# Kernel optimization log

Measured on AMD Instinct MI355X. Metric: run time of the kernel, lower is better.

Reference implementation:

```python
import jax, jax.numpy as jnp
from jax import lax
import numpy as np

B, N, G, K = 4, 1024, 128, 32
D_MODEL, DEPTH, CLS = 384, 12, 40
D_INNER, D_STATE, D_CONV, DT_RANK = 768, 16, 4, 24
EPS = 1e-5
BN_SCALE = 1.0 / float(np.sqrt(1.0 + EPS))  # eval BN, running_mean=0, running_var=1


def layernorm(x, w, b):
    mu = x.mean(-1, keepdims=True)
    var = ((x - mu) ** 2).mean(-1, keepdims=True)
    return (x - mu) * lax.rsqrt(var + EPS) * w + b


def bn_eval(x, g, b):
    return x * (g * BN_SCALE) + b


def fps(xyz, n):
    Bb, Nn, _ = xyz.shape
    first = jnp.zeros((Bb,), jnp.int32)

    def step(carry, _):
        dmin, last = carry
        p = jnp.take_along_axis(xyz, last[:, None, None], axis=1)  # B,1,3
        dmin = jnp.minimum(dmin, jnp.sum((xyz - p) ** 2, -1))
        nxt = jnp.argmax(dmin, -1).astype(jnp.int32)
        return (dmin, nxt), nxt

    _, rest = lax.scan(step, (jnp.full((Bb, Nn), 1e10, xyz.dtype), first), None, length=n - 1)
    return jnp.concatenate([first[None, :], rest], 0).T  # B,G


def group_points(xyz):
    idx = fps(xyz, G)
    center = jnp.take_along_axis(xyz, idx[:, :, None], axis=1)            # B,G,3
    d2 = jnp.sum((center[:, :, None, :] - xyz[:, None, :, :]) ** 2, -1)   # B,G,N
    _, knn = lax.top_k(-d2, K)                                            # B,G,K
    nb = jax.vmap(lambda p, i: p[i])(xyz, knn)                            # B,G,K,3
    return nb - center[:, :, None, :], center


def encoder(pg, w1, b1, g1, bb1, w2, b2, w3, b3, g2, bb2, w4, b4):
    Bb, Gg, Kk, _ = pg.shape
    f = pg.reshape(Bb * Gg, Kk, 3)
    f = jax.nn.relu(bn_eval(f @ w1.T + b1, g1, bb1))                      # BG,K,128
    f = f @ w2.T + b2                                                     # BG,K,256
    fg = f.max(1, keepdims=True)
    f = jnp.concatenate([jnp.broadcast_to(fg, f.shape), f], -1)           # BG,K,512
    f = jax.nn.relu(bn_eval(f @ w3.T + b3, g2, bb2))
    f = f @ w4.T + b4
    return f.max(1).reshape(Bb, Gg, -1)                                   # B,G,C


def mamba_mixer(x, ipw, cw, cb, xpw, dpw, dpb, A_log, Dp, opw):
    L = x.shape[1]
    xz = x @ ipw.T                                                        # B,L,2*Di
    u, z = jnp.split(xz, 2, -1)
    up = jnp.pad(u, ((0, 0), (D_CONV - 1, 0), (0, 0)))                    # causal depthwise conv
    u = sum(up[:, k:k + L, :] * cw[:, k] for k in range(D_CONV)) + cb
    u = jax.nn.silu(u)
    xdb = u @ xpw.T
    dt, Bm, Cm = jnp.split(xdb, [DT_RANK, DT_RANK + D_STATE], -1)
    dt = jax.nn.softplus(dt @ dpw.T + dpb)                                # B,L,Di
    A = -jnp.exp(A_log)                                                   # Di,Ds

    def step(h, inp):
        dt_t, B_t, C_t, u_t = inp
        h = jnp.exp(dt_t[:, :, None] * A) * h + (dt_t * u_t)[:, :, None] * B_t[:, None, :]
        return h, jnp.einsum('bds,bs->bd', h, C_t)

    h0 = jnp.zeros((x.shape[0], D_INNER, D_STATE), x.dtype)
    _, ys = lax.scan(step, h0, (dt.swapaxes(0, 1), Bm.swapaxes(0, 1), Cm.swapaxes(0, 1), u.swapaxes(0, 1)))
    y = ys.swapaxes(0, 1) + u * Dp
    return (y * jax.nn.silu(z)) @ opw.T


def forward(pts, enc_w1, enc_b1, enc_bn1_g, enc_bn1_b, enc_w2, enc_b2, enc_w3, enc_b3,
            enc_bn2_g, enc_bn2_b, enc_w4, enc_b4, pos_w1, pos_b1, pos_w2, pos_b2,
            ln_w, ln_b, in_proj_w, conv_w, conv_b, x_proj_w, dt_proj_w, dt_proj_b,
            A_log, D_param, out_proj_w, normf_w, normf_b, norm_w, norm_b,
            head_w1, head_b1, head_bn1_g, head_bn1_b, head_w2, head_b2,
            head_bn2_g, head_bn2_b, head_w3, head_b3):
    nb, center = group_points(pts)
    tok = encoder(nb, enc_w1, enc_b1, enc_bn1_g, enc_bn1_b, enc_w2, enc_b2,
                  enc_w3, enc_b3, enc_bn2_g, enc_bn2_b, enc_w4, enc_b4)    # B,G,384
    pos = jax.nn.gelu(center @ pos_w1.T + pos_b1, approximate=False) @ pos_w2.T + pos_b2

    # PointMamba token reordering: sort by center x, y, z and concatenate -> L = 3G
    toks, poss = [], []
    for ax in range(3):
        o = jnp.argsort(center[:, :, ax], axis=-1)[:, :, None]
        toks.append(jnp.take_along_axis(tok, o, axis=1))
        poss.append(jnp.take_along_axis(pos, o, axis=1))
    tok = jnp.concatenate(toks, 1)
    pos = jnp.concatenate(poss, 1)

    h = tok + pos
    res = jnp.zeros_like(h)

    def layer_step(carry, p):
        h, res = carry
        lnw, lnb, ipw, cw, cb, xpw, dpw, dpb, Al, Dp, opw = p
        res = h + res
        x = layernorm(res, lnw, lnb)
        h = mamba_mixer(x, ipw, cw, cb, xpw, dpw, dpb, Al, Dp, opw)
        return (h, res), None

    (h, res), _ = lax.scan(layer_step, (h, res),
                           (ln_w, ln_b, in_proj_w, conv_w, conv_b, x_proj_w,
                            dt_proj_w, dt_proj_b, A_log, D_param, out_proj_w))
    x = layernorm(h + res, normf_w, normf_b)   # MixerModel.norm_f
    x = layernorm(x, norm_w, norm_b)           # PointMamba.norm
    feat = x.mean(1)                           # B,384
    h1 = jax.nn.relu(bn_eval(feat @ head_w1.T + head_b1, head_bn1_g, head_bn1_b))
    h2 = jax.nn.relu(bn_eval(h1 @ head_w2.T + head_b2, head_bn2_g, head_bn2_b))
    return h2 @ head_w3.T + head_b3            # B,CLS


def setup_inputs():
    key = jax.random.key(0)
    ks = iter(jax.random.split(key, 64))

    def rn(shape, s=0.02):
        return jax.random.normal(next(ks), shape, jnp.float32) * s

    inp = dict(
        pts=jax.random.normal(next(ks), (B, N, 3), jnp.float32),
        enc_w1=rn((128, 3), 0.1), enc_b1=jnp.zeros((128,)),
        enc_bn1_g=jnp.ones((128,)), enc_bn1_b=jnp.zeros((128,)),
        enc_w2=rn((256, 128), 0.05), enc_b2=jnp.zeros((256,)),
        enc_w3=rn((512, 512), 0.05), enc_b3=jnp.zeros((512,)),
        enc_bn2_g=jnp.ones((512,)), enc_bn2_b=jnp.zeros((512,)),
        enc_w4=rn((D_MODEL, 512), 0.05), enc_b4=jnp.zeros((D_MODEL,)),
        pos_w1=rn((128, 3), 0.1), pos_b1=jnp.zeros((128,)),
        pos_w2=rn((D_MODEL, 128), 0.05), pos_b2=jnp.zeros((D_MODEL,)),
        ln_w=jnp.ones((DEPTH, D_MODEL)), ln_b=jnp.zeros((DEPTH, D_MODEL)),
        in_proj_w=rn((DEPTH, 2 * D_INNER, D_MODEL)),
        conv_w=rn((DEPTH, D_INNER, D_CONV), 0.2), conv_b=jnp.zeros((DEPTH, D_INNER)),
        x_proj_w=rn((DEPTH, DT_RANK + 2 * D_STATE, D_INNER)),
        dt_proj_w=rn((DEPTH, D_INNER, DT_RANK), 0.1),
        dt_proj_b=jnp.full((DEPTH, D_INNER), -4.6, jnp.float32),
        A_log=jnp.broadcast_to(jnp.log(jnp.arange(1, D_STATE + 1, dtype=jnp.float32)),
                               (DEPTH, D_INNER, D_STATE)).copy(),
        D_param=jnp.ones((DEPTH, D_INNER)),
        out_proj_w=rn((DEPTH, D_MODEL, D_INNER)),
        normf_w=jnp.ones((D_MODEL,)), normf_b=jnp.zeros((D_MODEL,)),
        norm_w=jnp.ones((D_MODEL,)), norm_b=jnp.zeros((D_MODEL,)),
        head_w1=rn((256, D_MODEL), 0.05), head_b1=jnp.zeros((256,)),
        head_bn1_g=jnp.ones((256,)), head_bn1_b=jnp.zeros((256,)),
        head_w2=rn((256, 256), 0.05), head_b2=jnp.zeros((256,)),
        head_bn2_g=jnp.ones((256,)), head_bn2_b=jnp.zeros((256,)),
        head_w3=rn((CLS, 256), 0.05), head_b3=jnp.zeros((CLS,)),
    )
    return inp


def reference(pts, enc_w1, enc_b1, enc_bn1_g, enc_bn1_b, enc_w2, enc_b2, enc_w3, enc_b3,
              enc_bn2_g, enc_bn2_b, enc_w4, enc_b4, pos_w1, pos_b1, pos_w2, pos_b2,
              ln_w, ln_b, in_proj_w, conv_w, conv_b, x_proj_w, dt_proj_w, dt_proj_b,
              A_log, D_param, out_proj_w, normf_w, normf_b, norm_w, norm_b,
              head_w1, head_b1, head_bn1_g, head_bn1_b, head_w2, head_b2,
              head_bn2_g, head_bn2_b, head_w3, head_b3):
    return forward(pts, enc_w1, enc_b1, enc_bn1_g, enc_bn1_b, enc_w2, enc_b2, enc_w3, enc_b3,
                   enc_bn2_g, enc_bn2_b, enc_w4, enc_b4, pos_w1, pos_b1, pos_w2, pos_b2,
                   ln_w, ln_b, in_proj_w, conv_w, conv_b, x_proj_w, dt_proj_w, dt_proj_b,
                   A_log, D_param, out_proj_w, normf_w, normf_b, norm_w, norm_b,
                   head_w1, head_b1, head_bn1_g, head_bn1_b, head_w2, head_b2,
                   head_bn2_g, head_bn2_b, head_w3, head_b3)
```

## Files before the change

### kernel.cpp

```cpp
#include <hip/hip_runtime.h>
#include <hip/hip_bf16.h>

using bf16 = __hip_bfloat16;
using short8  = __attribute__((ext_vector_type(8))) short;
using floatx4 = __attribute__((ext_vector_type(4))) float;
using ull = unsigned long long;

constexpr int Bn = 4, Np = 1024, Gn = 128, Kn = 32;
constexpr int DM = 384, DEPTH = 12, CLSn = 40;
constexpr int DI = 768, DSt = 16, DTR = 24;
constexpr int Ln = 384;
constexpr int NCH = 12, CHS = 32;
constexpr int CHB = 8,  NCB = 48;
constexpr int XDBS = 1536*56;
constexpr int MC = 4096;
constexpr float EPSf = 1e-5f;
constexpr float BNS = 0.99999500003749968752f;
constexpr float LOG2E = 1.4426950408889634f;

static __device__ __forceinline__ short f2bf(float f){
  bf16 h = __float2bfloat16(f);
  return *reinterpret_cast<short*>(&h);
}
static __device__ __forceinline__ float fsig(float x){ return 1.f/(1.f + __expf(-x)); }
static __device__ __forceinline__ float fsoftplus(float x){
  return fmaxf(x, 0.f) + __logf(1.f + __expf(-fabsf(x)));
}
static __device__ __forceinline__ ull umax64(ull a, ull b){ return a > b ? a : b; }

template<int CTRL>
static __device__ __forceinline__ int dppmov(int x){
  return __builtin_amdgcn_update_dpp(0, x, CTRL, 0xF, 0xF, true);
}
static __device__ __forceinline__ ull redmax64(ull key){
  #define RSTEP(CTRL) { \
    int hi = (int)(unsigned)(key >> 32), lo = (int)(unsigned)key; \
    int h2 = dppmov<CTRL>(hi), l2 = dppmov<CTRL>(lo); \
    ull k2 = ((ull)(unsigned)h2 << 32) | (unsigned)l2; \
    if (k2 > key) key = k2; }
  RSTEP(0x111) RSTEP(0x112) RSTEP(0x114) RSTEP(0x118) RSTEP(0x142) RSTEP(0x143)
  #undef RSTEP
  return key;
}

__global__ __launch_bounds__(256) void front_kernel(const float* __restrict__ pts,
    float* __restrict__ center,
    const float* __restrict__ s0, const float* __restrict__ s1,
    const float* __restrict__ s2, const float* __restrict__ s3,
    const float* __restrict__ s4, const float* __restrict__ s5,
    bf16* __restrict__ dst){
  __shared__ float4 P[1024];
  __shared__ ull red[2][4];
  if (blockIdx.x >= Bn){
    long i = ((long)(blockIdx.x - Bn)*256 + threadIdx.x)*4;
    if (i >= 11624448L) return;
    const float* s; long off;
    if      (i <  7077888L){ s = s0; off = 0L; }
// ... 587 lines not shown
  for (int i = 0; i < 6; ++i){ int c = ln + 64*i; float t = hr[c] + rr[c]; rr[c] = t; v[i] = t; s += t; }
  #pragma unroll
  for (int o = 32; o > 0; o >>= 1) s += __shfl_xor(s, o);
  float mu = s * (1.f/DM);
  float q = 0.f;
  #pragma unroll
  for (int i = 0; i < 6; ++i){ float d = v[i] - mu; q += d*d; }
  #pragma unroll
  for (int o = 32; o > 0; o >>= 1) q += __shfl_xor(q, o);
  float rstd = rsqrtf(q * (1.f/DM) + EPSf);
  #pragma unroll
  for (int i = 0; i < 6; ++i){ int c = ln + 64*i;
    xr[c] = __float2bfloat16((v[i]-mu)*rstd*w[c] + bias[c]); }
}

__global__ __launch_bounds__(256) void scanA_big(const float* __restrict__ xz,
    const float* __restrict__ xdbp, int nks,
    const float* __restrict__ cw, const float* __restrict__ cb,
    const float* __restrict__ dpw, const float* __restrict__ dpb,
    const float* __restrict__ A_log,
    float* __restrict__ SB_S, float* __restrict__ SB_dt,
    float* __restrict__ xdbR){
  __shared__ float sRow[CHB*56];
  int blk = blockIdx.x;
  int c = blk % NCB; int bd = blk / NCB; int dch = bd % 3; int b = bd / 3;
  int t = threadIdx.x; int d = dch*256 + t;
  int l0 = c*CHB;
  for (int i = t; i < CHB*56; i += 256){
    size_t base = ((size_t)(b*Ln + l0))*56 + i;
    float s = xdbp[base];
    for (int k = 1; k < nks; ++k) s += xdbp[(size_t)k*XDBS + base];
    sRow[i] = s;
    if (dch == 0) xdbR[base] = s;
  }
  float xv[CHB+3];
  #pragma unroll
  for (int j = 0; j < 3; ++j){
    int ll = l0 - 3 + j;
    xv[j] = (ll >= 0) ? xz[((size_t)(b*Ln + ll))*1536 + d] : 0.f;
  }
  const float* xp = xz + ((size_t)(b*Ln + l0))*1536 + d;
  #pragma unroll
  for (int i = 0; i < CHB; ++i) xv[3+i] = xp[(size_t)i*1536];
  float cw0 = cw[d*4+0], cw1 = cw[d*4+1], cw2 = cw[d*4+2], cw3 = cw[d*4+3];
  float cbv = cb[d];
  float uu[CHB];
  #pragma unroll
  for (int i = 0; i < CHB; ++i){
    float v = xv[i]*cw0 + xv[i+1]*cw1 + xv[i+2]*cw2 + xv[i+3]*cw3 + cbv;
    uu[i] = v * fsig(v);
  }
  float w[DTR];
  const float* wp = dpw + (size_t)d*DTR;
  #pragma unroll
  for (int j = 0; j < DTR; ++j) w[j] = wp[j];
  float a2[DSt], h[DSt];
  const float* ap = A_log + (size_t)d*DSt;
  #pragma unroll
  for (int s = 0; s < DSt; ++s){ a2[s] = -__expf(ap[s]) * LOG2E; h[s] = 0.f; }
  float dbias = dpb[d];
  float sumdt = 0.f;
  __syncthreads();
  for (int i = 0; i < CHB; ++i){
    int ro = i*56;
    float dtr = dbias;
    #pragma unroll
    for (int j = 0; j < DTR; ++j) dtr += w[j] * sRow[ro + j];
    float dtv = fsoftplus(dtr);
    sumdt += dtv;
    float du = dtv * uu[i];
    #pragma unroll
    for (int s = 0; s < DSt; ++s)
      h[s] = exp2f(dtv * a2[s]) * h[s] + du * sRow[ro + 24 + s];
  }
  size_t sb = ((size_t)blk*256 + t)*16;
  #pragma unroll
  for (int s = 0; s < DSt; ++s) SB_S[sb + s] = h[s];
  SB_dt[(size_t)blk*256 + t] = sumdt;
}

__global__ __launch_bounds__(256) void prefix_kernel(const float* __restrict__ A_log,
    const float* __restrict__ SB_S, const float* __restrict__ SB_dt,
    float* __restrict__ H0){
  int bb = blockIdx.x;
  int bd = bb >> 4;
  int dch = bd % 3;
  int tt = threadIdx.x;
  int tloc = tt >> 4, s = tt & 15;
  int t = (bb & 15)*16 + tloc;
  int d = dch*256 + t;
  float a2 = -__expf(A_log[(size_t)d*DSt + s]) * LOG2E;
  float H = 0.f;
  size_t tb = ((size_t)bd*NCB)*256 + t;
  for (int c = 0; c < NCB; ++c){
    size_t base = (tb + (size_t)c*256)*16 + s;
    H0[base] = H;
    float sd = SB_dt[tb + (size_t)c*256];
    H = exp2f(sd * a2) * H + SB_S[base];
  }
}

__global__ __launch_bounds__(256) void scanB_big(const float* __restrict__ xz,
    const float* __restrict__ xdbR,
    const float* __restrict__ cw, const float* __restrict__ cb,
    const float* __restrict__ dpw, const float* __restrict__ dpb,
    const float* __restrict__ A_log, const float* __restrict__ Dp,
    const float* __restrict__ H0, bf16* __restrict__ yb){
  __shared__ float sRow[CHB*56];
  int blk = blockIdx.x;
  int c = blk % NCB; int bd = blk / NCB; int dch = bd % 3; int b = bd / 3;
  int t = threadIdx.x; int d = dch*256 + t;
  int l0 = c*CHB;
  for (int i = t; i < CHB*56; i += 256)
    sRow[i] = xdbR[((size_t)(b*Ln + l0))*56 + i];
  float xv[CHB+3];
  #pragma unroll
  for (int j = 0; j < 3; ++j){
    int ll = l0 - 3 + j;
    xv[j] = (ll >= 0) ? xz[((size_t)(b*Ln + ll))*1536 + d] : 0.f;
  }
  const float* xp = xz + ((size_t)(b*Ln + l0))*1536 + d;
  #pragma unroll
  for (int i = 0; i < CHB; ++i) xv[3+i] = xp[(size_t)i*1536];
  float cw0 = cw[d*4+0], cw1 = cw[d*4+1], cw2 = cw[d*4+2], cw3 = cw[d*4+3];
  float cbv = cb[d];
  float uu[CHB];
  #pragma unroll
  for (int i = 0; i < CHB; ++i){
    float v = xv[i]*cw0 + xv[i+1]*cw1 + xv[i+2]*cw2 + xv[i+3]*cw3 + cbv;
    uu[i] = v * fsig(v);
  }
  float w[DTR];
  const float* wp = dpw + (size_t)d*DTR;
  #pragma unroll
  for (int j = 0; j < DTR; ++j) w[j] = wp[j];
  float a2[DSt], h[DSt];
  const float* ap = A_log + (size_t)d*DSt;
  #pragma unroll
  for (int s = 0; s < DSt; ++s) a2[s] = -__expf(ap[s]) * LOG2E;
  size_t hbase = (((size_t)bd*NCB + c)*256 + t)*16;
  #pragma unroll
  for (int s = 0; s < DSt; ++s) h[s] = H0[hbase + s];
  float dbias = dpb[d];
  float Dd = Dp[d];
  const float* zrow = xz + ((size_t)(b*Ln + l0))*1536 + 768 + d;
  bf16* ybr = yb + ((size_t)(b*Ln + l0))*DI + d;
  __syncthreads();
  for (int i = 0; i < CHB; ++i){
    int ro = i*56;
    float dtr = dbias;
    #pragma unroll
    for (int j = 0; j < DTR; ++j) dtr += w[j] * sRow[ro + j];
    float dtv = fsoftplus(dtr);
    float u = uu[i];
    float du = dtv * u;
    float yv = 0.f;
    #pragma unroll
    for (int s = 0; s < DSt; ++s){
      h[s] = exp2f(dtv * a2[s]) * h[s] + du * sRow[ro + 24 + s];
      yv += h[s] * sRow[ro + 40 + s];
    }
    float yfull = yv + u*Dd;
    float zv = zrow[(size_t)i*1536];
    ybr[(size_t)i*DI] = __float2bfloat16(yfull * (zv * fsig(zv)));
  }
}

__global__ __launch_bounds__(256) void scanA_kernel(const float* __restrict__ xz,
                                                    const float* __restrict__ xdbp, int nks,
                                                    const float* __restrict__ cw,
                                                    const float* __restrict__ cb,
                                                    const float* __restrict__ dpw,
                                                    const float* __restrict__ dpb,
                                                    const float* __restrict__ A_log,
                                                    float* __restrict__ SB_S,
                                                    float* __restrict__ SB_dt,
                                                    float* __restrict__ BND){
  __shared__ float sRow[CHS*56];
  __shared__ float sU[CHS*256];
  int blk = blockIdx.x;
  int c = blk % NCH; int bd = blk / NCH; int dch = bd % 3; int b = bd / 3;
  int t = threadIdx.x; int d = dch*256 + t;
// ... 199 lines not shown
    h1[t] = fmaxf(a, 0.f);
  }
  __syncthreads();
  {
    float a = b2[t];
    #pragma unroll 4
    for (int j = 0; j < 256; ++j) a += w2[(size_t)t*256 + j] * h1[j];
    a = a * (g2[t] * BNS) + bb2[t];
    h2[t] = fmaxf(a, 0.f);
  }
  __syncthreads();
  if (t < CLSn){
    float a = b3[t];
    for (int j = 0; j < 256; ++j) a += w3[(size_t)t*256 + j] * h2[j];
    out[b*CLSn + t] = a;
  }
}

extern "C" void kernel_launch(void* const* d_in, const int* in_sizes, int n_in,
                              void* d_out, int out_size, void* d_ws, size_t ws_size,
                              hipStream_t stream) {
  if (n_in < 42) return;
  if (out_size < Bn*CLSn) return;
  constexpr size_t WS_FLOATS = 3919936;
  if (ws_size < WS_FLOATS * sizeof(float)) return;
  constexpr size_t MIDF = 5812224;
  constexpr size_t BIGF = 9437184;
  const bool mid = ws_size >= (WS_FLOATS + MIDF) * sizeof(float);
  const bool big = ws_size >= (WS_FLOATS + MIDF + BIGF) * sizeof(float);

// ... 22 lines not shown
  const float* head_w3   = (const float*)d_in[40]; const float* head_b3   = (const float*)d_in[41];

  float* ws = (float*)d_ws;
  float* hb   = ws;
  float* resb = ws + 589824;
  float* U    = ws + 1179648;
  float* center = U;
  float* nb     = U + 1536;
  float* tok    = U + 50688;
  int*   order  = (int*)(U + 247296);
  bf16*  F3b_s  = (bf16*)(U + 262144);
  bf16*  F3c_s  = (bf16*)(U + 1310720);
  float* xz   = U;
  float* xdb  = U + 2359296;
  bf16*  xb   = (bf16*)(U + 2445312);
  float* SBdt = U + 2445312;
  float* BND  = U + 2482176;
  float* SBS  = hb;
  float* xf   = U;
  float* featp = U + 589824;
  float* WB = ws + WS_FLOATS;
  bf16* wb_ip = (bf16*)WB;
  bf16* wb_op = (bf16*)(WB + 3538944);
  bf16* wb_xp = (bf16*)(WB + 5308416);
  bf16* wb_e2 = (bf16*)(WB + 5566464);
  bf16* wb_e3 = (bf16*)(WB + 5582848);
  bf16* wb_e4 = (bf16*)(WB + 5713920);
  float* BIGB = WB + MIDF;
  bf16*  F3bB = (bf16*)BIGB;
  bf16*  F3cB = (bf16*)(BIGB + 4194304);
  float* xdbp_b = BIGB;
  float* xdbR   = BIGB + 1032192;
  bf16*  yb     = (bf16*)(BIGB + 1118208);
  float* SBS_b  = BIGB + 1708032;
  float* H0b    = BIGB + 4067328;
  float* SBdt_b = BIGB + 6426624;

  front_kernel<<<mid ? (Bn + 11352) : Bn, 256, 0, stream>>>(pts, center,
      in_proj_w, out_proj_w, x_proj_w, enc_w2, enc_w3, enc_w4, (bf16*)WB);
  knn_kernel<<<Bn*Gn, 256, 0, stream>>>(pts, center, nb);

  if (big){
    enc2_kernel<bf16><<<dim3(256,2), 256, 0, stream>>>(nb, enc_w1, enc_b1,
        enc_bn1_g, enc_bn1_b, wb_e2, enc_b2, F3bB);
    gemm_mfma128<bf16,bf16,1,bf16,0><<<dim3(256,4), 256, 0, stream>>>(F3bB, 512,
        wb_e3, enc_b3, enc_bn2_g, enc_bn2_b, F3cB, 512, 16384, 512, 512);
    gemm_mfma128<bf16,bf16,0,float,2><<<dim3(256,3), 256, 0, stream>>>(F3cB, 512,
        wb_e4, enc_b4, nullptr, nullptr, (float*)tok, DM, 16384, 384, 512);
  } else {
    for (int b = 0; b < Bn; ++b){
      const float* nbc = nb + (size_t)b*MC*3;
// ... 7 lines not shown
            wb_e4, enc_b4, nullptr, nullptr, (float*)tokc, DM, MC, 384, 512);
      } else {
        enc2_kernel<float><<<dim3(64,2), 256, 0, stream>>>(nbc, enc_w1, enc_b1,
            enc_bn1_g, enc_bn1_b, enc_w2, enc_b2, F3b_s);
        gemm_mfma128<bf16,float,1,bf16,0><<<dim3(64,4), 256, 0, stream>>>(F3b_s, 512,
            enc_w3, enc_b3, enc_bn2_g, enc_bn2_b, F3c_s, 512, MC, 512, 512);
        gemm_mfma128<bf16,float,0,float,2><<<dim3(64,3), 256, 0, stream>>>(F3c_s, 512,
            enc_w4, enc_b4, nullptr, nullptr, (float*)tokc, DM, MC, 384, 512);
      }
    }
  }

  pos_sort_kernel<<<Bn*Gn + Bn*3, 128, 0, stream>>>(center, pos_w1, pos_b1,
      pos_w2, pos_b2, tok, order);

  const int nks = big ? 12 : 1;
  float* xdbp = big ? xdbp_b : xdb;

  for (int l = 0; l < DEPTH; ++l){
    const float* lnw  = ln_w      + (size_t)l*DM;
    const float* lnb  = ln_b      + (size_t)l*DM;
    const float* ipw  = in_proj_w + (size_t)l*1536*DM;
    const float* cw   = conv_w    + (size_t)l*DI*4;
    const float* cb   = conv_b    + (size_t)l*DI;
    const float* xpw  = x_proj_w  + (size_t)l*56*DI;
    const float* dpw  = dt_proj_w + (size_t)l*DI*DTR;
    const float* dpb  = dt_proj_b + (size_t)l*DI;
    const float* Alg  = A_log     + (size_t)l*DI*DSt;
    const float* Dpar = D_param   + (size_t)l*DI;
    const float* opw  = out_proj_w+ (size_t)l*DM*DI;

    if (l == 0)
      ln_res_first<<<Bn*Ln/4, 256, 0, stream>>>(tok, order, resb, xb, lnw, lnb);
    else
      ln_res_kernel<<<Bn*Ln/4, 256, 0, stream>>>(hb, resb, xb, lnw, lnb);
    if (mid){
      gemm_mfma128<bf16,bf16,0,float,0><<<dim3(24,12), 256, 0, stream>>>(xb, DM,
          wb_ip + (size_t)l*1536*DM, nullptr, nullptr, nullptr, xz, 1536, Bn*Ln, 1536, DM);
      xproj_kernel<bf16><<<dim3(24, nks), 256, 0, stream>>>(xz,
          wb_xp + (size_t)l*56*DI, cw, cb, xdbp, DI/nks);
    } else {
      gemm_mfma128<bf16,float,0,float,0><<<dim3(24,12), 256, 0, stream>>>(xb, DM, ipw,
          nullptr, nullptr, nullptr, xz, 1536, Bn*Ln, 1536, DM);
      xproj_kernel<float><<<dim3(24, nks), 256, 0, stream>>>(xz, xpw, cw, cb, xdbp, DI/nks);
    }
    if (big){
      scanA_big<<<Bn*3*NCB, 256, 0, stream>>>(xz, xdbp, nks, cw, cb,
          dpw, dpb, Alg, SBS_b, SBdt_b, xdbR);
      prefix_kernel<<<Bn*3*16, 256, 0, stream>>>(Alg, SBS_b, SBdt_b, H0b);
      scanB_big<<<Bn*3*NCB, 256, 0, stream>>>(xz, xdbR, cw, cb,
          dpw, dpb, Alg, Dpar, H0b, yb);
      gemm_mfma128<bf16,bf16,0,float,0><<<dim3(24,3), 256, 0, stream>>>(yb, DI,
          wb_op + (size_t)l*DM*DI, nullptr, nullptr, nullptr, hb, DM, Bn*Ln, 384, DI);
    } else {
      scanA_kernel<<<Bn*3*NCH, 256, 0, stream>>>(xz, xdbp, nks, cw, cb,
          dpw, dpb, Alg, SBS, SBdt, BND);
      scanB_kernel<<<Bn*3*NCH, 256, 0, stream>>>(xz, xdbp, nks, cw, cb,
          dpw, dpb, Alg, Dpar, SBS, SBdt, BND);
      if (mid){
        gemm_mfma64<float,bf16,0,1><<<dim3(24,6), 256, 0, stream>>>(xz, 1536,
            wb_op + (size_t)l*DM*DI, nullptr, xz, nullptr, hb, DM, Bn*Ln, DM, DI);
      } else {
        gemm_mfma64<float,float,0,1><<<dim3(24,6), 256, 0, stream>>>(xz, 1536, opw,
            nullptr, xz, nullptr, hb, DM, Bn*Ln, DM, DI);
      }
    }
  }

  final_ln_kernel<<<Bn*Ln/4, 256, 0, stream>>>(hb, resb, normf_w, normf_b, norm_w, norm_b, xf);
  mean_kernel<<<Bn*4, 384, 0, stream>>>(xf, featp);
  head_mlp<<<Bn, 256, 0, stream>>>(featp, head_w1, head_b1, head_bn1_g, head_bn1_b,
                                   head_w2, head_b2, head_bn2_g, head_bn2_b,
                                   head_w3, head_b3, (float*)d_out);
}
```

Baseline: 1.479 ms.

## Fuse all Mamba layers and head into one persistent kernel with grid barriers

When the big-workspace path is taken, the per-layer launches (layernorm, in_proj GEMM, x_proj, scanA, prefix, scanB, out_proj) and the final LN, mean and head are replaced by a single persistent kernel. It runs on 256 blocks and separates phases with a software grid barrier built on atomics. The aim is to remove roughly 80+ kernel launch gaps. In exchange, each phase has less parallelism than its own launch had, the GEMM tiles are simpler and unpipelined, barrier spin cost is added, and correctness depends on all 256 blocks being co-resident.

Result: slower. 5.359 ms (+262.4%).

```diff
diff --git a/kernel.cpp b/kernel.cpp
--- a/kernel.cpp
+++ b/kernel.cpp
@@ -14,6 +14,7 @@
 constexpr int CHB = 8,  NCB = 48;
 constexpr int XDBS = 1536*56;
 constexpr int MC = 4096;
+constexpr int MGRID = 256;
 constexpr float EPSf = 1e-5f;
 constexpr float BNS = 0.99999500003749968752f;
 constexpr float LOG2E = 1.4426950408889634f;
@@ -41,6 +42,25 @@
   RSTEP(0x111) RSTEP(0x112) RSTEP(0x114) RSTEP(0x118) RSTEP(0x142) RSTEP(0x143)
   #undef RSTEP
   return key;
+}
+
+static __device__ __forceinline__ void gbar(int* cnt, int* gen){
+  __syncthreads();
+  if (threadIdx.x == 0){
+    __threadfence();
+    int g = __hip_atomic_load(gen, __ATOMIC_RELAXED, __HIP_MEMORY_SCOPE_AGENT);
+    int v = __hip_atomic_fetch_add(cnt, 1, __ATOMIC_ACQ_REL, __HIP_MEMORY_SCOPE_AGENT);
+    if (v == (int)gridDim.x - 1){
+      __hip_atomic_store(cnt, 0, __ATOMIC_RELAXED, __HIP_MEMORY_SCOPE_AGENT);
+      __hip_atomic_fetch_add(gen, 1, __ATOMIC_ACQ_REL, __HIP_MEMORY_SCOPE_AGENT);
+    } else {
+      while (__hip_atomic_load(gen, __ATOMIC_ACQUIRE, __HIP_MEMORY_SCOPE_AGENT) == g){
+        __builtin_amdgcn_s_sleep(8);
+      }
+    }
+    __threadfence();
+  }
+  __syncthreads();
 }
 
 __global__ __launch_bounds__(256) void front_kernel(const float* __restrict__ pts,
@@ -658,158 +678,6 @@
     xr[c] = __float2bfloat16((v[i]-mu)*rstd*w[c] + bias[c]); }
 }
 
-__global__ __launch_bounds__(256) void scanA_big(const float* __restrict__ xz,
-    const float* __restrict__ xdbp, int nks,
-    const float* __restrict__ cw, const float* __restrict__ cb,
-    const float* __restrict__ dpw, const float* __restrict__ dpb,
-    const float* __restrict__ A_log,
-    float* __restrict__ SB_S, float* __restrict__ SB_dt,
-    float* __restrict__ xdbR){
-  __shared__ float sRow[CHB*56];
-  int blk = blockIdx.x;
-  int c = blk % NCB; int bd = blk / NCB; int dch = bd % 3; int b = bd / 3;
-  int t = threadIdx.x; int d = dch*256 + t;
-  int l0 = c*CHB;
-  for (int i = t; i < CHB*56; i += 256){
-    size_t base = ((size_t)(b*Ln + l0))*56 + i;
-    float s = xdbp[base];
-    for (int k = 1; k < nks; ++k) s += xdbp[(size_t)k*XDBS + base];
-    sRow[i] = s;
-    if (dch == 0) xdbR[base] = s;
-  }
-  float xv[CHB+3];
-  #pragma unroll
-  for (int j = 0; j < 3; ++j){
-    int ll = l0 - 3 + j;
-    xv[j] = (ll >= 0) ? xz[((size_t)(b*Ln + ll))*1536 + d] : 0.f;
-  }
-  const float* xp = xz + ((size_t)(b*Ln + l0))*1536 + d;
-  #pragma unroll
-  for (int i = 0; i < CHB; ++i) xv[3+i] = xp[(size_t)i*1536];
-  float cw0 = cw[d*4+0], cw1 = cw[d*4+1], cw2 = cw[d*4+2], cw3 = cw[d*4+3];
-  float cbv = cb[d];
-  float uu[CHB];
-  #pragma unroll
-  for (int i = 0; i < CHB; ++i){
-    float v = xv[i]*cw0 + xv[i+1]*cw1 + xv[i+2]*cw2 + xv[i+3]*cw3 + cbv;
-    uu[i] = v * fsig(v);
-  }
-  float w[DTR];
-  const float* wp = dpw + (size_t)d*DTR;
-  #pragma unroll
-  for (int j = 0; j < DTR; ++j) w[j] = wp[j];
-  float a2[DSt], h[DSt];
-  const float* ap = A_log + (size_t)d*DSt;
-  #pragma unroll
-  for (int s = 0; s < DSt; ++s){ a2[s] = -__expf(ap[s]) * LOG2E; h[s] = 0.f; }
-  float dbias = dpb[d];
-  float sumdt = 0.f;
-  __syncthreads();
-  for (int i = 0; i < CHB; ++i){
-    int ro = i*56;
-    float dtr = dbias;
-    #pragma unroll
-    for (int j = 0; j < DTR; ++j) dtr += w[j] * sRow[ro + j];
-    float dtv = fsoftplus(dtr);
-    sumdt += dtv;
-    float du = dtv * uu[i];
-    #pragma unroll
-    for (int s = 0; s < DSt; ++s)
-      h[s] = exp2f(dtv * a2[s]) * h[s] + du * sRow[ro + 24 + s];
-  }
-  size_t sb = ((size_t)blk*256 + t)*16;
-  #pragma unroll
-  for (int s = 0; s < DSt; ++s) SB_S[sb + s] = h[s];
-  SB_dt[(size_t)blk*256 + t] = sumdt;
-}
-
-__global__ __launch_bounds__(256) void prefix_kernel(const float* __restrict__ A_log,
-    const float* __restrict__ SB_S, const float* __restrict__ SB_dt,
-    float* __restrict__ H0){
-  int bb = blockIdx.x;
-  int bd = bb >> 4;
-  int dch = bd % 3;
-  int tt = threadIdx.x;
-  int tloc = tt >> 4, s = tt & 15;
-  int t = (bb & 15)*16 + tloc;
-  int d = dch*256 + t;
-  float a2 = -__expf(A_log[(size_t)d*DSt + s]) * LOG2E;
-  float H = 0.f;
-  size_t tb = ((size_t)bd*NCB)*256 + t;
-  for (int c = 0; c < NCB; ++c){
-    size_t base = (tb + (size_t)c*256)*16 + s;
-    H0[base] = H;
-    float sd = SB_dt[tb + (size_t)c*256];
-    H = exp2f(sd * a2) * H + SB_S[base];
-  }
-}
-
-__global__ __launch_bounds__(256) void scanB_big(const float* __restrict__ xz,
-    const float* __restrict__ xdbR,
-    const float* __restrict__ cw, const float* __restrict__ cb,
-    const float* __restrict__ dpw, const float* __restrict__ dpb,
-    const float* __restrict__ A_log, const float* __restrict__ Dp,
-    const float* __restrict__ H0, bf16* __restrict__ yb){
-  __shared__ float sRow[CHB*56];
-  int blk = blockIdx.x;
-  int c = blk % NCB; int bd = blk / NCB; int dch = bd % 3; int b = bd / 3;
-  int t = threadIdx.x; int d = dch*256 + t;
-  int l0 = c*CHB;
-  for (int i = t; i < CHB*56; i += 256)
-    sRow[i] = xdbR[((size_t)(b*Ln + l0))*56 + i];
-  float xv[CHB+3];
-  #pragma unroll
-  for (int j = 0; j < 3; ++j){
-    int ll = l0 - 3 + j;
-    xv[j] = (ll >= 0) ? xz[((size_t)(b*Ln + ll))*1536 + d] : 0.f;
-  }
-  const float* xp = xz + ((size_t)(b*Ln + l0))*1536 + d;
-  #pragma unroll
-  for (int i = 0; i < CHB; ++i) xv[3+i] = xp[(size_t)i*1536];
-  float cw0 = cw[d*4+0], cw1 = cw[d*4+1], cw2 = cw[d*4+2], cw3 = cw[d*4+3];
-  float cbv = cb[d];
-  float uu[CHB];
-  #pragma unroll
-  for (int i = 0; i < CHB; ++i){
-    float v = xv[i]*cw0 + xv[i+1]*cw1 + xv[i+2]*cw2 + xv[i+3]*cw3 + cbv;
-    uu[i] = v * fsig(v);
-  }
-  float w[DTR];
-  const float* wp = dpw + (size_t)d*DTR;
-  #pragma unroll
-  for (int j = 0; j < DTR; ++j) w[j] = wp[j];
-  float a2[DSt], h[DSt];
-  const float* ap = A_log + (size_t)d*DSt;
-  #pragma unroll
-  for (int s = 0; s < DSt; ++s) a2[s] = -__expf(ap[s]) * LOG2E;
-  size_t hbase = (((size_t)bd*NCB + c)*256 + t)*16;
-  #pragma unroll
-  for (int s = 0; s < DSt; ++s) h[s] = H0[hbase + s];
-  float dbias = dpb[d];
-  float Dd = Dp[d];
-  const float* zrow = xz + ((size_t)(b*Ln + l0))*1536 + 768 + d;
-  bf16* ybr = yb + ((size_t)(b*Ln + l0))*DI + d;
-  __syncthreads();
-  for (int i = 0; i < CHB; ++i){
-    int ro = i*56;
-    float dtr = dbias;
-    #pragma unroll
-    for (int j = 0; j < DTR; ++j) dtr += w[j] * sRow[ro + j];
-    float dtv = fsoftplus(dtr);
-    float u = uu[i];
-    float du = dtv * u;
-    float yv = 0.f;
-    #pragma unroll
-    for (int s = 0; s < DSt; ++s){
-      h[s] = exp2f(dtv * a2[s]) * h[s] + du * sRow[ro + 24 + s];
-      yv += h[s] * sRow[ro + 40 + s];
-    }
-    float yfull = yv + u*Dd;
-    float zv = zrow[(size_t)i*1536];
-    ybr[(size_t)i*DI] = __float2bfloat16(yfull * (zv * fsig(zv)));
-  }
-}
-
 __global__ __launch_bounds__(256) void scanA_kernel(const float* __restrict__ xz,
                                                     const float* __restrict__ xdbp, int nks,
                                                     const float* __restrict__ cw,
@@ -1039,6 +907,464 @@
     float a = b3[t];
     for (int j = 0; j < 256; ++j) a += w3[(size_t)t*256 + j] * h2[j];
     out[b*CLSn + t] = a;
+  }
+}
+
+__global__ __launch_bounds__(256) void mega_layers(
+    const float* __restrict__ tok, const int* __restrict__ order,
+    float* __restrict__ hb, float* __restrict__ resb,
+    bf16* __restrict__ xb, float* __restrict__ xz,
+    float* __restrict__ xdbp, float* __restrict__ xdbR,
+    bf16* __restrict__ yb, float* __restrict__ SBS,
+    float* __restrict__ SBdt, float* __restrict__ H0,
+    int* __restrict__ syncp,
+    const float* __restrict__ lnw_all, const float* __restrict__ lnb_all,
+    const bf16* __restrict__ wip, const bf16* __restrict__ wxp,
+    const bf16* __restrict__ wop,
+    const float* __restrict__ cw_all, const float* __restrict__ cb_all,
+    const float* __restrict__ dpw_all, const float* __restrict__ dpb_all,
+    const float* __restrict__ Alog_all, const float* __restrict__ Dp_all,
+    const float* __restrict__ normf_w, const float* __restrict__ normf_b,
+    const float* __restrict__ norm_w, const float* __restrict__ norm_b,
+    float* __restrict__ xf, float* __restrict__ featp,
+    const float* __restrict__ hw1, const float* __restrict__ hbi1,
+    const float* __restrict__ hg1, const float* __restrict__ hbb1,
+    const float* __restrict__ hw2, const float* __restrict__ hbi2,
+    const float* __restrict__ hg2, const float* __restrict__ hbb2,
+    const float* __restrict__ hw3, const float* __restrict__ hbi3,
+    float* __restrict__ outp)
+{
+  __shared__ __align__(16) short As[64*72];
+  __shared__ __align__(16) short Ws[128*72];
+  int* cnt = syncp;
+  int* gen = syncp + 1;
+  int t = threadIdx.x;
+  int w = t >> 6, lane = t & 63, m16 = lane & 15, q = lane >> 4;
+  int row = t >> 2, kseg = (t & 3) * 16;
+  int row2 = t >> 1, kseg2 = (t & 1) * 32;
+
+  for (int l = 0; l < DEPTH; ++l){
+    const float* lnw  = lnw_all + (size_t)l*DM;
+    const float* lnb  = lnb_all + (size_t)l*DM;
+    const bf16*  ipw  = wip + (size_t)l*1536*DM;
+    const bf16*  xpw  = wxp + (size_t)l*56*DI;
+    const bf16*  opw  = wop + (size_t)l*DM*DI;
+    const float* cw   = cw_all + (size_t)l*DI*4;
+    const float* cb   = cb_all + (size_t)l*DI;
+    const float* dpw  = dpw_all + (size_t)l*DI*DTR;
+    const float* dpb  = dpb_all + (size_t)l*DI;
+    const float* Alg  = Alog_all + (size_t)l*DI*DSt;
+    const float* Dpar = Dp_all + (size_t)l*DI;
+
+    for (int wu = blockIdx.x; wu < Bn*Ln/4; wu += gridDim.x){
+      int wv = w, ln = lane;
+      int tokid = wu*4 + wv;
+      float* rr = resb + (size_t)tokid*DM;
+      bf16* xr = xb + (size_t)tokid*DM;
+      float v[6]; float s = 0.f;
+      if (l == 0){
+        int b = tokid / Ln;
+        int src = order[tokid];
+        src = min(max(src, 0), Gn-1);
+        const float* hr = tok + ((size_t)(b*Gn + src))*DM;
+        #pragma unroll
+        for (int i = 0; i < 6; ++i){ int c = ln + 64*i; float tv = hr[c]; rr[c] = tv; v[i] = tv; s += tv; }
+      } else {
+        const float* hr = hb + (size_t)tokid*DM;
+        #pragma unroll
+        for (int i = 0; i < 6; ++i){ int c = ln + 64*i; float tv = hr[c] + rr[c]; rr[c] = tv; v[i] = tv; s += tv; }
+      }
+      #pragma unroll
+      for (int o = 32; o > 0; o >>= 1) s += __shfl_xor(s, o);
+      float mu = s * (1.f/DM);
+      float qq = 0.f;
+      #pragma unroll
+      for (int i = 0; i < 6; ++i){ float d = v[i] - mu; qq += d*d; }
+      #pragma unroll
+      for (int o = 32; o > 0; o >>= 1) qq += __shfl_xor(qq, o);
+      float rstd = rsqrtf(qq * (1.f/DM) + EPSf);
+      #pragma unroll
+      for (int i = 0; i < 6; ++i){ int c = ln + 64*i;
+        xr[c] = __float2bfloat16((v[i]-mu)*rstd*lnw[c] + lnb[c]); }
+    }
+    gbar(cnt, gen);
+
+    for (int wu = blockIdx.x; wu < 288; wu += gridDim.x){
+      int bm = (wu % 24)*64, bn = (wu / 24)*128;
+      floatx4 acc[8] = {};
+      for (int k0 = 0; k0 < DM; k0 += 64){
+        const short* Ar = (const short*)xb + (size_t)(bm + row)*DM + k0 + kseg;
+        *(short8*)&As[row*72 + kseg]     = *(const short8*)Ar;
+        *(short8*)&As[row*72 + kseg + 8] = *(const short8*)(Ar + 8);
+        {
+          int n = bn + row2;
+          const short* Wr = (const short*)ipw + (size_t)n*DM + k0 + kseg2;
+          *(short8*)&Ws[row2*72 + kseg2]      = *(const short8*)Wr;
+          *(short8*)&Ws[row2*72 + kseg2 + 8]  = *(const short8*)(Wr + 8);
+          *(short8*)&Ws[row2*72 + kseg2 + 16] = *(const short8*)(Wr + 16);
+          *(short8*)&Ws[row2*72 + kseg2 + 24] = *(const short8*)(Wr + 24);
+        }
+        __syncthreads();
+        short8 af0 = *(const short8*)&As[(w*16 + m16)*72 + q*8];
+        short8 af1 = *(const short8*)&As[(w*16 + m16)*72 + 32 + q*8];
+        #pragma unroll
+        for (int j = 0; j < 8; ++j){
+          short8 b0 = *(const short8*)&Ws[(j*16 + m16)*72 + q*8];
+          acc[j] = __builtin_amdgcn_mfma_f32_16x16x32_bf16(af0, b0, acc[j], 0, 0, 0);
+          short8 b1 = *(const short8*)&Ws[(j*16 + m16)*72 + 32 + q*8];
+          acc[j] = __builtin_amdgcn_mfma_f32_16x16x32_bf16(af1, b1, acc[j], 0, 0, 0);
+        }
+        __syncthreads();
+      }
+      #pragma unroll
+      for (int j = 0; j < 8; ++j){
+        int n = bn + j*16 + m16;
+        #pragma unroll
+        for (int r = 0; r < 4; ++r){
+          int m = bm + w*16 + q*4 + r;
+          xz[(size_t)m*1536 + n] = acc[j][r];
+        }
+      }
+    }
+    gbar(cnt, gen);
+
+    for (int wu = blockIdx.x; wu < 288; wu += gridDim.x){
+      int bm = (wu % 24)*64;
+      int ks = wu / 24;
+      int m = bm + row;
+      int lpos = m % Ln;
+      int k0 = ks * 64;
+      floatx4 acc[4] = {};
+      const float4 z4 = make_float4(0.f,0.f,0.f,0.f);
+      {
+        int ch = k0 + kseg;
+        const float* base = xz + (size_t)m*1536 + ch;
+        float x0[16], x1[16], x2[16], x3[16];
+        #pragma unroll
+        for (int j4 = 0; j4 < 4; ++j4){
+          *(float4*)&x3[j4*4] = *(const float4*)(base + j4*4);
+          *(float4*)&x2[j4*4] = (lpos >= 1) ? *(const float4*)(base - 1536 + j4*4) : z4;
+          *(float4*)&x1[j4*4] = (lpos >= 2) ? *(const float4*)(base - 2*1536 + j4*4) : z4;
+          *(float4*)&x0[j4*4] = (lpos >= 3) ? *(const float4*)(base - 3*1536 + j4*4) : z4;
+        }
+        short* dstp = &As[row*72 + kseg];
+        #pragma unroll
+        for (int j = 0; j < 16; ++j){
+          float4 wv4 = *(const float4*)(cw + (size_t)(ch + j)*4);
+          float v = x0[j]*wv4.x + x1[j]*wv4.y + x2[j]*wv4.z + x3[j]*wv4.w + cb[ch + j];
+          v = v * fsig(v);
+          dstp[j] = f2bf(v);
+        }
+        {
+          int n = row;
+          short8 v0, v1;
+          #pragma unroll
+          for (int j = 0; j < 8; ++j){ v0[j] = 0; v1[j] = 0; }
+          if (n < 56){
+            const short* Wr = (const short*)xpw + (size_t)n*DI + k0 + kseg;
+            v0 = *(const short8*)Wr;
+            v1 = *(const short8*)(Wr + 8);
+          }
+          *(short8*)&Ws[row*72 + kseg]     = v0;
+          *(short8*)&Ws[row*72 + kseg + 8] = v1;
+        }
+        __syncthreads();
+        short8 af0 = *(const short8*)&As[(w*16 + m16)*72 + q*8];
+        short8 af1 = *(const short8*)&As[(w*16 + m16)*72 + 32 + q*8];
+        #pragma unroll
+        for (int j = 0; j < 4; ++j){
+          short8 b0 = *(const short8*)&Ws[(j*16 + m16)*72 + q*8];
+          acc[j] = __builtin_amdgcn_mfma_f32_16x16x32_bf16(af0, b0, acc[j], 0, 0, 0);
+          short8 b1 = *(const short8*)&Ws[(j*16 + m16)*72 + 32 + q*8];
+          acc[j] = __builtin_amdgcn_mfma_f32_16x16x32_bf16(af1, b1, acc[j], 0, 0, 0);
+        }
+        __syncthreads();
+      }
+      float* C = xdbp + (size_t)ks * XDBS;
+      #pragma unroll
+      for (int j = 0; j < 4; ++j){
+        int n = j*16 + m16;
+        if (n < 56){
+          #pragma unroll
+          for (int r = 0; r < 4; ++r){
+            int mm = bm + w*16 + q*4 + r;
+            C[(size_t)mm*56 + n] = acc[j][r];
+          }
+        }
+      }
+    }
+    gbar(cnt, gen);
+
+    {
+      float* sRow = (float*)As;
+      for (int wu = blockIdx.x; wu < Bn*3*NCB; wu += gridDim.x){
+        int c = wu % NCB; int bd = wu / NCB; int dch = bd % 3; int b = bd / 3;
+        int d = dch*256 + t;
+        int l0 = c*CHB;
+        for (int i = t; i < CHB*56; i += 256){
+          size_t base = ((size_t)(b*Ln + l0))*56 + i;
+          float s = xdbp[base];
+          for (int k = 1; k < 12; ++k) s += xdbp[(size_t)k*XDBS + base];
+          sRow[i] = s;
+          if (dch == 0) xdbR[base] = s;
+        }
+        float xv[CHB+3];
+        #pragma unroll
+        for (int j = 0; j < 3; ++j){
+          int ll = l0 - 3 + j;
+          xv[j] = (ll >= 0) ? xz[((size_t)(b*Ln + ll))*1536 + d] : 0.f;
+        }
+        const float* xp = xz + ((size_t)(b*Ln + l0))*1536 + d;
+        #pragma unroll
+        for (int i = 0; i < CHB; ++i) xv[3+i] = xp[(size_t)i*1536];
+        float cw0 = cw[d*4+0], cw1 = cw[d*4+1], cw2 = cw[d*4+2], cw3 = cw[d*4+3];
+        float cbv = cb[d];
+        float uu[CHB];
+        #pragma unroll
+        for (int i = 0; i < CHB; ++i){
+          float v = xv[i]*cw0 + xv[i+1]*cw1 + xv[i+2]*cw2 + xv[i+3]*cw3 + cbv;
+          uu[i] = v * fsig(v);
+        }
+        float wv[DTR];
+        const float* wp = dpw + (size_t)d*DTR;
+        #pragma unroll
+        for (int j = 0; j < DTR; ++j) wv[j] = wp[j];
+        float a2[DSt], h[DSt];
+        const float* ap = Alg + (size_t)d*DSt;
+        #pragma unroll
+        for (int s = 0; s < DSt; ++s){ a2[s] = -__expf(ap[s]) * LOG2E; h[s] = 0.f; }
+        float dbias = dpb[d];
+        float sumdt = 0.f;
+        __syncthreads();
+        for (int i = 0; i < CHB; ++i){
+          int ro = i*56;
+          float dtr = dbias;
+          #pragma unroll
+          for (int j = 0; j < DTR; ++j) dtr += wv[j] * sRow[ro + j];
+          float dtv = fsoftplus(dtr);
+          sumdt += dtv;
+          float du = dtv * uu[i];
+          #pragma unroll
+          for (int s = 0; s < DSt; ++s)
+            h[s] = exp2f(dtv * a2[s]) * h[s] + du * sRow[ro + 24 + s];
+        }
+        size_t sb = ((size_t)wu*256 + t)*16;
+        #pragma unroll
+        for (int s = 0; s < DSt; ++s) SBS[sb + s] = h[s];
+        SBdt[(size_t)wu*256 + t] = sumdt;
+        __syncthreads();
+      }
+    }
+    gbar(cnt, gen);
+
+    for (int wu = blockIdx.x; wu < Bn*3*16; wu += gridDim.x){
+      int bd = wu >> 4;
+      int dch = bd % 3;
+      int tloc = t >> 4, s = t & 15;
+      int tcol = (wu & 15)*16 + tloc;
+      int d = dch*256 + tcol;
+      float a2 = -__expf(Alg[(size_t)d*DSt + s]) * LOG2E;
+      float H = 0.f;
+      size_t tb = ((size_t)bd*NCB)*256 + tcol;
+      for (int c = 0; c < NCB; ++c){
+        size_t base = (tb + (size_t)c*256)*16 + s;
+        H0[base] = H;
+        float sd = SBdt[tb + (size_t)c*256];
+        H = exp2f(sd * a2) * H + SBS[base];
+      }
+    }
+    gbar(cnt, gen);
+
+    {
+      float* sRow = (float*)As;
+      for (int wu = blockIdx.x; wu < Bn*3*NCB; wu += gridDim.x){
+        int c = wu % NCB; int bd = wu / NCB; int dch = bd % 3; int b = bd / 3;
+        int d = dch*256 + t;
+        int l0 = c*CHB;
+        for (int i = t; i < CHB*56; i += 256)
+          sRow[i] = xdbR[((size_t)(b*Ln + l0))*56 + i];
+        float xv[CHB+3];
+        #pragma unroll
+        for (int j = 0; j < 3; ++j){
+          int ll = l0 - 3 + j;
+          xv[j] = (ll >= 0) ? xz[((size_t)(b*Ln + ll))*1536 + d] : 0.f;
+        }
+        const float* xp = xz + ((size_t)(b*Ln + l0))*1536 + d;
+        #pragma unroll
+        for (int i = 0; i < CHB; ++i) xv[3+i] = xp[(size_t)i*1536];
+        float cw0 = cw[d*4+0], cw1 = cw[d*4+1], cw2 = cw[d*4+2], cw3 = cw[d*4+3];
+        float cbv = cb[d];
+        float uu[CHB];
+        #pragma unroll
+        for (int i = 0; i < CHB; ++i){
+          float v = xv[i]*cw0 + xv[i+1]*cw1 + xv[i+2]*cw2 + xv[i+3]*cw3 + cbv;
+          uu[i] = v * fsig(v);
+        }
+        float wv[DTR];
+        const float* wp = dpw + (size_t)d*DTR;
+        #pragma unroll
+        for (int j = 0; j < DTR; ++j) wv[j] = wp[j];
+        float a2[DSt], h[DSt];
+        const float* ap = Alg + (size_t)d*DSt;
+        #pragma unroll
+        for (int s = 0; s < DSt; ++s) a2[s] = -__expf(ap[s]) * LOG2E;
+        size_t hbase = ((size_t)wu*256 + t)*16;
+        #pragma unroll
+        for (int s = 0; s < DSt; ++s) h[s] = H0[hbase + s];
+        float dbias = dpb[d];
+        float Dd = Dpar[d];
+        const float* zrow = xz + ((size_t)(b*Ln + l0))*1536 + 768 + d;
+        bf16* ybr = yb + ((size_t)(b*Ln + l0))*DI + d;
+        __syncthreads();
+        for (int i = 0; i < CHB; ++i){
+          int ro = i*56;
+          float dtr = dbias;
+          #pragma unroll
+          for (int j = 0; j < DTR; ++j) dtr += wv[j] * sRow[ro + j];
+          float dtv = fsoftplus(dtr);
+          float u = uu[i];
+          float du = dtv * u;
+          float yv = 0.f;
+          #pragma unroll
+          for (int s = 0; s < DSt; ++s){
+            h[s] = exp2f(dtv * a2[s]) * h[s] + du * sRow[ro + 24 + s];
+            yv += h[s] * sRow[ro + 40 + s];
+          }
+          float yfull = yv + u*Dd;
+          float zv = zrow[(size_t)i*1536];
+          ybr[(size_t)i*DI] = __float2bfloat16(yfull * (zv * fsig(zv)));
+        }
+        __syncthreads();
+      }
+    }
+    gbar(cnt, gen);
+
+    for (int wu = blockIdx.x; wu < 72; wu += gridDim.x){
+      int bm = (wu % 24)*64, bn = (wu / 24)*128;
+      floatx4 acc[8] = {};
+      for (int k0 = 0; k0 < DI; k0 += 64){
+        const short* Ar = (const short*)yb + (size_t)(bm + row)*DI + k0 + kseg;
+        *(short8*)&As[row*72 + kseg]     = *(const short8*)Ar;
+        *(short8*)&As[row*72 + kseg + 8] = *(const short8*)(Ar + 8);
+        {
+          int n = bn + row2;
+          const short* Wr = (const short*)opw + (size_t)n*DI + k0 + kseg2;
+          *(short8*)&Ws[row2*72 + kseg2]      = *(const short8*)Wr;
+          *(short8*)&Ws[row2*72 + kseg2 + 8]  = *(const short8*)(Wr + 8);
+          *(short8*)&Ws[row2*72 + kseg2 + 16] = *(const short8*)(Wr + 16);
+          *(short8*)&Ws[row2*72 + kseg2 + 24] = *(const short8*)(Wr + 24);
+        }
+        __syncthreads();
+        short8 af0 = *(const short8*)&As[(w*16 + m16)*72 + q*8];
+        short8 af1 = *(const short8*)&As[(w*16 + m16)*72 + 32 + q*8];
+        #pragma unroll
+        for (int j = 0; j < 8; ++j){
+          short8 b0 = *(const short8*)&Ws[(j*16 + m16)*72 + q*8];
+          acc[j] = __builtin_amdgcn_mfma_f32_16x16x32_bf16(af0, b0, acc[j], 0, 0, 0);
+          short8 b1 = *(const short8*)&Ws[(j*16 + m16)*72 + 32 + q*8];
+          acc[j] = __builtin_amdgcn_mfma_f32_16x16x32_bf16(af1, b1, acc[j], 0, 0, 0);
+        }
+        __syncthreads();
+      }
+      #pragma unroll
+      for (int j = 0; j < 8; ++j){
+        int n = bn + j*16 + m16;
+        #pragma unroll
+        for (int r = 0; r < 4; ++r){
+          int m = bm + w*16 + q*4 + r;
+          hb[(size_t)m*DM + n] = acc[j][r];
+        }
+      }
+    }
+    gbar(cnt, gen);
+  }
+
+  for (int wu = blockIdx.x; wu < Bn*Ln/4; wu += gridDim.x){
+    int wv = w, ln = lane;
+    int tokid = wu*4 + wv;
+    const float* hr = hb + (size_t)tokid*DM;
+    const float* rr = resb + (size_t)tokid*DM;
+    float* xr = xf + (size_t)tokid*DM;
+    float v[6]; float s = 0.f;
+    #pragma unroll
+    for (int i = 0; i < 6; ++i){ int c = ln + 64*i; v[i] = hr[c] + rr[c]; s += v[i]; }
+    #pragma unroll
+    for (int o = 32; o > 0; o >>= 1) s += __shfl_xor(s, o);
+    float mu = s * (1.f/DM); float qq = 0.f;
+    #pragma unroll
+    for (int i = 0; i < 6; ++i){ float dd = v[i]-mu; qq += dd*dd; }
+    #pragma unroll
+    for (int o = 32; o > 0; o >>= 1) qq += __shfl_xor(qq, o);
+    float rstd = rsqrtf(qq * (1.f/DM) + EPSf);
+    float u[6]; float s2 = 0.f;
+    #pragma unroll
+    for (int i = 0; i < 6; ++i){ int c = ln + 64*i; u[i] = (v[i]-mu)*rstd*normf_w[c] + normf_b[c]; s2 += u[i]; }
+    #pragma unroll
+    for (int o = 32; o > 0; o >>= 1) s2 += __shfl_xor(s2, o);
+    float mu2 = s2 * (1.f/DM); float q2 = 0.f;
+    #pragma unroll
+    for (int i = 0; i < 6; ++i){ float dd = u[i]-mu2; q2 += dd*dd; }
+    #pragma unroll
+    for (int o = 32; o > 0; o >>= 1) q2 += __shfl_xor(q2, o);
+    float rstd2 = rsqrtf(q2 * (1.f/DM) + EPSf);
+    #pragma unroll
+    for (int i = 0; i < 6; ++i){ int c = ln + 64*i; xr[c] = (u[i]-mu2)*rstd2*norm_w[c] + norm_b[c]; }
+  }
+  gbar(cnt, gen);
+
+  for (int wu = blockIdx.x; wu < Bn*4; wu += gridDim.x){
+    int b = wu >> 2, g = wu & 3;
+    for (int c = t; c < DM; c += 256){
+      const float* xp = xf + ((size_t)(b*Ln + g*96))*DM + c;
+      float a0=0.f,a1=0.f,a2=0.f,a3=0.f,a4=0.f,a5=0.f,a6=0.f,a7=0.f;
+      for (int ll = 0; ll < 96; ll += 8){
+        a0 += xp[(size_t)(ll+0)*DM];
+        a1 += xp[(size_t)(ll+1)*DM];
+        a2 += xp[(size_t)(ll+2)*DM];
+        a3 += xp[(size_t)(ll+3)*DM];
+        a4 += xp[(size_t)(ll+4)*DM];
+        a5 += xp[(size_t)(ll+5)*DM];
+        a6 += xp[(size_t)(ll+6)*DM];
+        a7 += xp[(size_t)(ll+7)*DM];
+      }
+      featp[(size_t)wu*DM + c] = ((a0+a1)+(a2+a3)) + ((a4+a5)+(a6+a7));
+    }
+  }
+  gbar(cnt, gen);
+
+  {
+    float* shf = (float*)As;
+    float* sh1 = shf + DM;
+    float* sh2 = sh1 + 256;
+    for (int wu = blockIdx.x; wu < Bn; wu += gridDim.x){
+      for (int i = t; i < DM; i += 256){
+        shf[i] = (featp[(size_t)(wu*4+0)*DM + i] + featp[(size_t)(wu*4+1)*DM + i]
+                + featp[(size_t)(wu*4+2)*DM + i] + featp[(size_t)(wu*4+3)*DM + i]) * (1.f/Ln);
+      }
+      __syncthreads();
+      {
+        float a = hbi1[t];
+        #pragma unroll 4
+        for (int j = 0; j < DM; ++j) a += hw1[(size_t)t*DM + j] * shf[j];
+        a = a * (hg1[t] * BNS) + hbb1[t];
+        sh1[t] = fmaxf(a, 0.f);
+      }
+      __syncthreads();
+      {
+        float a = hbi2[t];
+        #pragma unroll 4
+        for (int j = 0; j < 256; ++j) a += hw2[(size_t)t*256 + j] * sh1[j];
+        a = a * (hg2[t] * BNS) + hbb2[t];
+        sh2[t] = fmaxf(a, 0.f);
+      }
+      __syncthreads();
+      if (t < CLSn){
+        float a = hbi3[t];
+        for (int j = 0; j < 256; ++j) a += hw3[(size_t)t*256 + j] * sh2[j];
+        outp[wu*CLSn + t] = a;
+      }
+      __syncthreads();
+    }
   }
 }
 
@@ -1091,9 +1417,9 @@
   float* xz   = U;
   float* xdb  = U + 2359296;
   bf16*  xb   = (bf16*)(U + 2445312);
-  float* SBdt = U + 2445312;
+  float* SBdt_s = U + 2445312;
   float* BND  = U + 2482176;
-  float* SBS  = hb;
+  float* SBS_sm = hb;
   float* xf   = U;
   float* featp = U + 589824;
   float* WB = ws + WS_FLOATS;
@@ -1112,6 +1438,7 @@
   float* SBS_b  = BIGB + 1708032;
   float* H0b    = BIGB + 4067328;
   float* SBdt_b = BIGB + 6426624;
+  int*   syncp  = (int*)(BIGB + 6600000);
 
   front_kernel<<<mid ? (Bn + 11352) : Bn, 256, 0, stream>>>(pts, center,
       in_proj_w, out_proj_w, x_proj_w, enc_w2, enc_w3, enc_w4, (bf16*)WB);
@@ -1149,49 +1476,48 @@
   pos_sort_kernel<<<Bn*Gn + Bn*3, 128, 0, stream>>>(center, pos_w1, pos_b1,
       pos_w2, pos_b2, tok, order);
 
-  const int nks = big ? 12 : 1;
-  float* xdbp = big ? xdbp_b : xdb;
-
-  for (int l = 0; l < DEPTH; ++l){
-    const float* lnw  = ln_w      + (size_t)l*DM;
-    const float* lnb  = ln_b      + (size_t)l*DM;
-    const float* ipw  = in_proj_w + (size_t)l*1536*DM;
-    const float* cw   = conv_w    + (size_t)l*DI*4;
-    const float* cb   = conv_b    + (size_t)l*DI;
-    const float* xpw  = x_proj_w  + (size_t)l*56*DI;
-    const float* dpw  = dt_proj_w + (size_t)l*DI*DTR;
-    const float* dpb  = dt_proj_b + (size_t)l*DI;
-    const float* Alg  = A_log     + (size_t)l*DI*DSt;
-    const float* Dpar = D_param   + (size_t)l*DI;
-    const float* opw  = out_proj_w+ (size_t)l*DM*DI;
-
-    if (l == 0)
-      ln_res_first<<<Bn*Ln/4, 256, 0, stream>>>(tok, order, resb, xb, lnw, lnb);
-    else
-      ln_res_kernel<<<Bn*Ln/4, 256, 0, stream>>>(hb, resb, xb, lnw, lnb);
-    if (mid){
-      gemm_mfma128<bf16,bf16,0,float,0><<<dim3(24,12), 256, 0, stream>>>(xb, DM,
-          wb_ip + (size_t)l*1536*DM, nullptr, nullptr, nullptr, xz, 1536, Bn*Ln, 1536, DM);
-      xproj_kernel<bf16><<<dim3(24, nks), 256, 0, stream>>>(xz,
-          wb_xp + (size_t)l*56*DI, cw, cb, xdbp, DI/nks);
-    } else {
-      gemm_mfma128<bf16,float,0,float,0><<<dim3(24,12), 256, 0, stream>>>(xb, DM, ipw,
-          nullptr, nullptr, nullptr, xz, 1536, Bn*Ln, 1536, DM);
-      xproj_kernel<float><<<dim3(24, nks), 256, 0, stream>>>(xz, xpw, cw, cb, xdbp, DI/nks);
-    }
-    if (big){
-      scanA_big<<<Bn*3*NCB, 256, 0, stream>>>(xz, xdbp, nks, cw, cb,
-          dpw, dpb, Alg, SBS_b, SBdt_b, xdbR);
-      prefix_kernel<<<Bn*3*16, 256, 0, stream>>>(Alg, SBS_b, SBdt_b, H0b);
-      scanB_big<<<Bn*3*NCB, 256, 0, stream>>>(xz, xdbR, cw, cb,
-          dpw, dpb, Alg, Dpar, H0b, yb);
-      gemm_mfma128<bf16,bf16,0,float,0><<<dim3(24,3), 256, 0, stream>>>(yb, DI,
-          wb_op + (size_t)l*DM*DI, nullptr, nullptr, nullptr, hb, DM, Bn*Ln, 384, DI);
-    } else {
-      scanA_kernel<<<Bn*3*NCH, 256, 0, stream>>>(xz, xdbp, nks, cw, cb,
-          dpw, dpb, Alg, SBS, SBdt, BND);
-      scanB_kernel<<<Bn*3*NCH, 256, 0, stream>>>(xz, xdbp, nks, cw, cb,
-          dpw, dpb, Alg, Dpar, SBS, SBdt, BND);
+  if (big){
+    hipMemsetAsync(syncp, 0, 16, stream);
+    mega_layers<<<MGRID, 256, 0, stream>>>(
+        tok, order, hb, resb, xb, xz, xdbp_b, xdbR, yb, SBS_b, SBdt_b, H0b,
+        syncp, ln_w, ln_b, wb_ip, wb_xp, wb_op,
+        conv_w, conv_b, dt_proj_w, dt_proj_b, A_log, D_param,
+        normf_w, normf_b, norm_w, norm_b, xf, featp,
+        head_w1, head_b1, head_bn1_g, head_bn1_b,
+        head_w2, head_b2, head_bn2_g, head_bn2_b,
+        head_w3, head_b3, (float*)d_out);
+  } else {
+    for (int l = 0; l < DEPTH; ++l){
+      const float* lnw  = ln_w      + (size_t)l*DM;
+      const float* lnb  = ln_b      + (size_t)l*DM;
+      const float* ipw  = in_proj_w + (size_t)l*1536*DM;
+      const float* cw   = conv_w    + (size_t)l*DI*4;
+      const float* cb   = conv_b    + (size_t)l*DI;
+      const float* xpw  = x_proj_w  + (size_t)l*56*DI;
+      const float* dpw  = dt_proj_w + (size_t)l*DI*DTR;
+      const float* dpb  = dt_proj_b + (size_t)l*DI;
+      const float* Alg  = A_log     + (size_t)l*DI*DSt;
+      const float* Dpar = D_param   + (size_t)l*DI;
+      const float* opw  = out_proj_w+ (size_t)l*DM*DI;
+
+      if (l == 0)
+        ln_res_first<<<Bn*Ln/4, 256, 0, stream>>>(tok, order, resb, xb, lnw, lnb);
+      else
+        ln_res_kernel<<<Bn*Ln/4, 256, 0, stream>>>(hb, resb, xb, lnw, lnb);
+      if (mid){
+        gemm_mfma128<bf16,bf16,0,float,0><<<dim3(24,12), 256, 0, stream>>>(xb, DM,
+            wb_ip + (size_t)l*1536*DM, nullptr, nullptr, nullptr, xz, 1536, Bn*Ln, 1536, DM);
+        xproj_kernel<bf16><<<dim3(24,1), 256, 0, stream>>>(xz,
+            wb_xp + (size_t)l*56*DI, cw, cb, xdb, DI);
+      } else {
+        gemm_mfma128<bf16,float,0,float,0><<<dim3(24,12), 256, 0, stream>>>(xb, DM, ipw,
+            nullptr, nullptr, nullptr, xz, 1536, Bn*Ln, 1536, DM);
+        xproj_kernel<float><<<dim3(24,1), 256, 0, stream>>>(xz, xpw, cw, cb, xdb, DI);
+      }
+      scanA_kernel<<<Bn*3*NCH, 256, 0, stream>>>(xz, xdb, 1, cw, cb,
+          dpw, dpb, Alg, SBS_sm, SBdt_s, BND);
+      scanB_kernel<<<Bn*3*NCH, 256, 0, stream>>>(xz, xdb, 1, cw, cb,
+          dpw, dpb, Alg, Dpar, SBS_sm, SBdt_s, BND);
       if (mid){
         gemm_mfma64<float,bf16,0,1><<<dim3(24,6), 256, 0, stream>>>(xz, 1536,
             wb_op + (size_t)l*DM*DI, nullptr, xz, nullptr, hb, DM, Bn*Ln, DM, DI);
@@ -1200,11 +1526,10 @@
             nullptr, xz, nullptr, hb, DM, Bn*Ln, DM, DI);
       }
     }
-  }
-
-  final_ln_kernel<<<Bn*Ln/4, 256, 0, stream>>>(hb, resb, normf_w, normf_b, norm_w, norm_b, xf);
-  mean_kernel<<<Bn*4, 384, 0, stream>>>(xf, featp);
-  head_mlp<<<Bn, 256, 0, stream>>>(featp, head_w1, head_b1, head_bn1_g, head_bn1_b,
-                                   head_w2, head_b2, head_bn2_g, head_bn2_b,
-                                   head_w3, head_b3, (float*)d_out);
-}
+    final_ln_kernel<<<Bn*Ln/4, 256, 0, stream>>>(hb, resb, normf_w, normf_b, norm_w, norm_b, xf);
+    mean_kernel<<<Bn*4, 384, 0, stream>>>(xf, featp);
+    head_mlp<<<Bn, 256, 0, stream>>>(featp, head_w1, head_b1, head_bn1_g, head_bn1_b,
+                                     head_w2, head_b2, head_bn2_g, head_bn2_b,
+                                     head_w3, head_b3, (float*)d_out);
+  }
+}
```
